# Optimization experiments

Hardware: AMD Instinct MI355X
Metric: run time of the kernel (lower is better)

## Reference

```python
import jax, jax.numpy as jnp
import numpy as np

D_PAIR = 128
D_BIAS = 128
N_HEAD = 4
D_HID = 32
B = 1
L = 384
EPS = 1e-5


def _layernorm(x, gamma, beta):
    m = jnp.mean(x, axis=-1, keepdims=True)
    v = jnp.var(x, axis=-1, keepdims=True)
    return (x - m) * jax.lax.rsqrt(v + EPS) * gamma + beta


def setup_inputs() -> dict:
    key = jax.random.key(0)
    ks = jax.random.split(key, 10)
    hd = N_HEAD * D_HID
    s = 0.02
    return {
        "pair": jax.random.normal(ks[0], (B, L, L, D_PAIR), jnp.float32),
        "bias": jax.random.normal(ks[1], (B, L, L, D_BIAS), jnp.float32),
        "gamma_p": jnp.ones((D_PAIR,), jnp.float32),
        "beta_p": jnp.zeros((D_PAIR,), jnp.float32),
        "gamma_b": jnp.ones((D_BIAS,), jnp.float32),
        "beta_b": jnp.zeros((D_BIAS,), jnp.float32),
        "Wq": jax.random.normal(ks[2], (D_PAIR, hd), jnp.float32) * s,
        "Wk": jax.random.normal(ks[3], (D_PAIR, hd), jnp.float32) * s,
        "Wv": jax.random.normal(ks[4], (D_PAIR, hd), jnp.float32) * s,
        "Wb": jax.random.normal(ks[5], (D_BIAS, N_HEAD), jnp.float32) * s,
        "Wg": jax.random.normal(ks[6], (D_PAIR, hd), jnp.float32) * s,
        "bg": jnp.ones((hd,), jnp.float32),
        "Wout": jax.random.normal(ks[7], (hd, D_PAIR), jnp.float32) * s,
        "bout": jnp.zeros((D_PAIR,), jnp.float32),
    }


def reference(pair, bias, gamma_p, beta_p, gamma_b, beta_b,
              Wq, Wk, Wv, Wb, Wg, bg, Wout, bout):
    h = Wb.shape[1]
    d = Wq.shape[1] // h
    Bn, Ln = pair.shape[:2]
    scaling = 1.0 / jnp.sqrt(jnp.asarray(d, pair.dtype))

    # is_row=True: attend along rows -> swap the two L axes
    pair_t = jnp.transpose(pair, (0, 2, 1, 3))
    bias_t = jnp.transpose(bias, (0, 2, 1, 3))

    pn = _layernorm(pair_t, gamma_p, beta_p)                     # [B,L,L,dp]
    q = (pn @ Wq).reshape(Bn, Ln, Ln, h, d) * scaling            # [B,n,i,h,d]
    k = (pn @ Wk).reshape(Bn, Ln, Ln, h, d) / Ln                 # [B,n,j,h,d]

    # mean-over-n biased axial attention logits: [B,i,j,h]
    attn = jnp.einsum('bnihk,bnjhk->bijh', q, k)
    attn = attn + _layernorm(bias_t, gamma_b, beta_b) @ Wb       # learned bias
    a = jax.nn.softmax(attn, axis=-2)                            # over j

    v = (pn @ Wv).reshape(Bn, Ln, Ln, h, d)                      # [B,n,j,h,d]
    o = jnp.einsum('bijh,bnjhd->bnihd', a, v).reshape(Bn, Ln, Ln, h * d)

    gate = jax.nn.sigmoid(pn @ Wg + bg)                          # [B,L,L,h*d]
    out = (gate * o) @ Wout + bout                               # [B,L,L,dp]

    return jnp.transpose(out, (0, 2, 1, 3))                      # undo is_row permute
```

## Files before the change

kernel.cpp:

```cpp
#include <hip/hip_runtime.h>

typedef unsigned short u16;
typedef unsigned int   u32;
typedef __attribute__((ext_vector_type(8))) short bf16x8;
typedef __attribute__((ext_vector_type(4))) float f32x4;

#define LL 384
#define DP 128
#define SZROW ((size_t)LL * LL)

#define SWZ(row, col) (((row) << 7) + (((((col) >> 3) ^ ((row) & 7)) << 3) | ((col) & 7)))

__device__ __forceinline__ u16 f2bf(float x) {
  u32 u = __builtin_bit_cast(u32, x);
  u = (u + 0x7FFFu + ((u >> 16) & 1u)) >> 16;
  return (u16)u;
}
__device__ __forceinline__ float bf2f(u16 h) {
  return __builtin_bit_cast(float, ((u32)h) << 16);
}
__device__ __forceinline__ uint2 pack4(float a, float b, float c, float d) {
  uint2 p;
  p.x = (u32)f2bf(a) | ((u32)f2bf(b) << 16);
  p.y = (u32)f2bf(c) | ((u32)f2bf(d) << 16);
  return p;
}


__global__ void k_prep(const float* __restrict__ Wq, const float* __restrict__ Wk,
                       const float* __restrict__ Wv, const float* __restrict__ Wg,
                       const float* __restrict__ Wout, u16* __restrict__ wbf) {
  int r = blockIdx.x, c = threadIdx.x, m = blockIdx.y;
  const float* W;
  float s = 1.0f;
  if (m == 0)      { W = Wq;  s = 0.17677669529663687f; }
  else if (m == 1) { W = Wk;  s = 1.0f / 384.0f; }
  else if (m == 2) { W = Wv; }
  else if (m == 3) { W = Wg; }
  else             { W = Wout; }
  wbf[m * DP * DP + r * DP + c] = f2bf(W[c * DP + r] * s);
}

template <int NS>
__device__ __forceinline__ void wave_gemm(const u16* __restrict__ W, const u16* pnl,
                                          int wave, int q, int r, f32x4 (&acc)[2][NS]) {
  const f32x4 FZ = {0.f, 0.f, 0.f, 0.f};
#pragma unroll
  for (int ms = 0; ms < 2; ++ms)
#pragma unroll
    for (int ns = 0; ns < NS; ++ns) acc[ms][ns] = FZ;
#pragma unroll
  for (int kc = 0; kc < 4; ++kc) {
    bf16x8 a0 = *(const bf16x8*)(W + (wave * 32 + r) * DP + kc * 32 + q * 8);
    bf16x8 a1 = *(const bf16x8*)(W + (wave * 32 + 16 + r) * DP + kc * 32 + q * 8);
#pragma unroll
    for (int ns = 0; ns < NS; ++ns) {
      bf16x8 b = *(const bf16x8*)(pnl + SWZ(ns * 16 + r, kc * 32 + q * 8));
      acc[0][ns] = __builtin_amdgcn_mfma_f32_16x16x32_bf16(a0, b, acc[0][ns], 0, 0, 0);
      acc[1][ns] = __builtin_amdgcn_mfma_f32_16x16x32_bf16(a1, b, acc[1][ns], 0, 0, 0);
    }
  }
}

__global__ __launch_bounds__(256) void k1_ln_proj(
    const float* __restrict__ pair, const float* __restrict__ gamma_p,
    const float* __restrict__ beta_p, const u16* __restrict__ wbf,
    const float* __restrict__ bg, u16* __restrict__ Qb, u16* __restrict__ Kb,
    u16* __restrict__ Vp, u16* __restrict__ Gtb) {
  __shared__ u16 pn[64 * 128];
  __shared__ u16 T[128 * 72];
  const int ib = blockIdx.x, n = blockIdx.y;
  const int tid = threadIdx.x;
  const int lane = tid & 63, wave = tid >> 6;
  const int q = lane >> 4, r = lane & 15;
  const int l32 = lane & 31, half = lane >> 5;
  const int c0 = l32 * 4;
  const float4 gm = *(const float4*)(gamma_p + c0);
  const float4 bt = *(const float4*)(beta_p + c0);

#pragma unroll
  for (int it = 0; it < 8; ++it) {
    const int il = it * 8 + wave * 2 + half;
    const float* rowp = pair + ((size_t)(ib * 64 + il) * LL + n) * DP + c0;
    float4 x = *(const float4*)rowp;
    float s1 = x.x + x.y + x.z + x.w;
    float s2 = x.x * x.x + x.y * x.y + x.z * x.z + x.w * x.w;
#pragma unroll
    for (int m = 16; m >= 1; m >>= 1) { s1 += __shfl_xor(s1, m); s2 += __shfl_xor(s2, m); }
    float mean = s1 * (1.0f / 128.0f);
    float rs = rsqrtf(s2 * (1.0f / 128.0f) - mean * mean + 1e-5f);
    *(uint2*)(&pn[SWZ(il, c0)]) =
        pack4((x.x - mean) * rs * gm.x + bt.x, (x.y - mean) * rs * gm.y + bt.y,
              (x.z - mean) * rs * gm.z + bt.z, (x.w - mean) * rs * gm.w + bt.w);
  }
  __syncthreads();

  f32x4 acc[2][4];

  wave_gemm<4>(wbf, pn, wave, q, r, acc);
#pragma unroll
  for (int ms = 0; ms < 2; ++ms) {
#pragma unroll
    for (int ns = 0; ns < 4; ++ns) {
      size_t base = (((size_t)n * 4 + wave) * LL + ib * 64 + ns * 16 + r) * 32 + ms * 16 + q * 4;
      *(uint2*)(Qb + base) = pack4(acc[ms][ns][0], acc[ms][ns][1], acc[ms][ns][2], acc[ms][ns][3]);
    }
  }
  wave_gemm<4>(wbf + DP * DP, pn, wave, q, r, acc);
#pragma unroll
  for (int ms = 0; ms < 2; ++ms) {
#pragma unroll
    for (int ns = 0; ns < 4; ++ns) {
      size_t base = (((size_t)n * 4 + wave) * LL + ib * 64 + ns * 16 + r) * 32 + ms * 16 + q * 4;
      *(uint2*)(Kb + base) = pack4(acc[ms][ns][0], acc[ms][ns][1], acc[ms][ns][2], acc[ms][ns][3]);
    }
  }
  wave_gemm<4>(wbf + 2 * DP * DP, pn, wave, q, r, acc);
#pragma unroll
  for (int ms = 0; ms < 2; ++ms)
#pragma unroll
    for (int ns = 0; ns < 4; ++ns)
#pragma unroll
      for (int reg = 0; reg < 4; ++reg)
        T[(wave * 32 + ms * 16 + q * 4 + reg) * 72 + ns * 16 + r] = f2bf(acc[ms][ns][reg]);
  __syncthreads();
#pragma unroll
  for (int kk = 0; kk < 2; ++kk) {
    u16* dst = Vp + ((size_t)n * 12 + ib * 2 + kk) * (128 * 32);
#pragma unroll
    for (int e = 0; e < 2; ++e) {
      int m = e * 256 + tid;
      int c = m >> 2, io = (m & 3) * 8;
      *(uint4*)(dst + c * 32 + io) = *(const uint4*)(T + c * 72 + kk * 32 + io);
    }
  }
  wave_gemm<4>(wbf + 3 * DP * DP, pn, wave, q, r, acc);
  __syncthreads();
#pragma unroll
  for (int ms = 0; ms < 2; ++ms) {
    f32x4 bgv = *(const f32x4*)(bg + wave * 32 + ms * 16 + q * 4);
#pragma unroll
    for (int ns = 0; ns < 4; ++ns)
#pragma unroll
      for (int reg = 0; reg < 4; ++reg) {
        float x = acc[ms][ns][reg] + bgv[reg];
        T[(wave * 32 + ms * 16 + q * 4 + reg) * 72 + ns * 16 + r] =
            f2bf(1.0f / (1.0f + __expf(-x)));
      }
  }
  __syncthreads();
#pragma unroll
  for (int it = 0; it < 4; ++it) {
    int c = it * 32 + (tid >> 3);
    int il2 = (tid & 7) * 8;
    *(uint4*)(Gtb + ((size_t)n * DP + c) * LL + ib * 64 + il2) =
        *(const uint4*)(T + c * 72 + il2);
  }
}

__global__ __launch_bounds__(256) void k2a_bias(
    const float* __restrict__ bias, const float* __restrict__ gamma_b,
    const float* __restrict__ beta_b, const float* __restrict__ Wb,
    float* __restrict__ part) {
  const int lane = threadIdx.x & 63, wave = threadIdx.x >> 6;
  const int l32 = lane & 31, half = lane >> 5;
  const int row = blockIdx.x * 8 + wave * 2 + half;
  const int i = row % LL, j = row / LL;
  const int c0 = l32 * 4;
  float4 x = *(const float4*)(bias + (size_t)row * DP + c0);
  float s1 = x.x + x.y + x.z + x.w;
  float s2 = x.x * x.x + x.y * x.y + x.z * x.z + x.w * x.w;
#pragma unroll
  for (int m = 16; m >= 1; m >>= 1) { s1 += __shfl_xor(s1, m); s2 += __shfl_xor(s2, m); }
  float mean = s1 * (1.0f / 128.0f);
  float rs = rsqrtf(s2 * (1.0f / 128.0f) - mean * mean + 1e-5f);
  const float4 gm = *(const float4*)(gamma_b + c0);
  const float4 bt = *(const float4*)(beta_b + c0);
  float y0 = (x.x - mean) * rs * gm.x + bt.x;
  float y1 = (x.y - mean) * rs * gm.y + bt.y;
  float y2 = (x.z - mean) * rs * gm.z + bt.z;
  float y3 = (x.w - mean) * rs * gm.w + bt.w;
  f32x4 w0 = *(const f32x4*)(Wb + (c0 + 0) * 4);
  f32x4 w1 = *(const f32x4*)(Wb + (c0 + 1) * 4);
  f32x4 w2 = *(const f32x4*)(Wb + (c0 + 2) * 4);
  f32x4 w3 = *(const f32x4*)(Wb + (c0 + 3) * 4);
  f32x4 pv = y0 * w0 + y1 * w1 + y2 * w2 + y3 * w3;
#pragma unroll
  for (int m = 16; m >= 1; m >>= 1) {
    pv[0] += __shfl_xor(pv[0], m); pv[1] += __shfl_xor(pv[1], m);
    pv[2] += __shfl_xor(pv[2], m); pv[3] += __shfl_xor(pv[3], m);
  }
  if (l32 == 0) {
    size_t o = (size_t)i * LL + j;
    part[(size_t)32 * SZROW + o] = pv[0];
    part[(size_t)33 * SZROW + o] = pv[1];
    part[(size_t)34 * SZROW + o] = pv[2];
    part[(size_t)35 * SZROW + o] = pv[3];
  }
}

__global__ __launch_bounds__(256) void k2b_qk(const u16* __restrict__ Qb,
                                              const u16* __restrict__ Kb,
                                              float* __restrict__ part) {
  const int it = blockIdx.y, jt = blockIdx.x >> 3, nc = blockIdx.x & 7;
  const int lane = threadIdx.x & 63, h = threadIdx.x >> 6;
  const int q = lane >> 4, r = lane & 15;
  const f32x4 FZ = {0.f, 0.f, 0.f, 0.f};
  f32x4 acc[3][3];
#pragma unroll
  for (int a = 0; a < 3; ++a)
#pragma unroll
    for (int b = 0; b < 3; ++b) acc[a][b] = FZ;
#pragma unroll 2
  for (int n = nc * 48; n < nc * 48 + 48; ++n) {
    const u16* Qp = Qb + (((size_t)n * 4 + h) * LL + it * 48 + r) * 32 + q * 8;
    const u16* Kp = Kb + (((size_t)n * 4 + h) * LL + jt * 48 + r) * 32 + q * 8;
    bf16x8 av[3], bv[3];
#pragma unroll
    for (int s = 0; s < 3; ++s) {
      av[s] = *(const bf16x8*)(Qp + s * 16 * 32);
      bv[s] = *(const bf16x8*)(Kp + s * 16 * 32);
    }
#pragma unroll
    for (int is = 0; is < 3; ++is)
#pragma unroll
      for (int js = 0; js < 3; ++js)
        acc[is][js] = __builtin_amdgcn_mfma_f32_16x16x32_bf16(av[is], bv[js], acc[is][js], 0, 0, 0);
  }
  float* dst = part + (size_t)(nc * 4 + h) * SZROW;
#pragma unroll
  for (int is = 0; is < 3; ++is)
#pragma unroll
    for (int js = 0; js < 3; ++js)
#pragma unroll
      for (int reg = 0; reg < 4; ++reg)
        dst[(size_t)(it * 48 + is * 16 + q * 4 + reg) * LL + jt * 48 + js * 16 + r] =
            acc[is][js][reg];
}

__global__ __launch_bounds__(384) void k3_softmax(const float* __restrict__ part,
                                                  u16* __restrict__ ap) {
  const int i = blockIdx.x, h = blockIdx.y, j = threadIdx.x;
  __shared__ float red[6];
  float l = 0.f;
#pragma unroll
  for (int c = 0; c < 9; ++c) l += part[(size_t)(c * 4 + h) * SZROW + (size_t)i * LL + j];
  float m = l;
#pragma unroll
  for (int s = 32; s >= 1; s >>= 1) m = fmaxf(m, __shfl_xor(m, s));
  const int wv = threadIdx.x >> 6;
  if ((threadIdx.x & 63) == 0) red[wv] = m;
  __syncthreads();
  m = fmaxf(fmaxf(fmaxf(red[0], red[1]), fmaxf(red[2], red[3])), fmaxf(red[4], red[5]));
  float e = __expf(l - m);
  float s = e;
#pragma unroll
  for (int t = 32; t >= 1; t >>= 1) s += __shfl_xor(s, t);
  __syncthreads();
  if ((threadIdx.x & 63) == 0) red[wv] = s;
  __syncthreads();
  s = red[0] + red[1] + red[2] + red[3] + red[4] + red[5];
  ap[(((size_t)h * 12 + (j >> 5)) * LL + i) * 32 + (j & 31)] = f2bf(e / s);
}

__global__ __launch_bounds__(256) void k4_out(
    const u16* __restrict__ ap, const u16* __restrict__ Vp,
    const u16* __restrict__ Gtb, const u16* __restrict__ Wot,
    const float* __restrict__ bout, float* __restrict__ out) {
  __shared__ __align__(16) char smem[64 * 132 * 4];
  u16*   go = (u16*)smem;
  float* O  = (float*)smem;
  const int n = blockIdx.x, ib = blockIdx.y;
  const int tid = threadIdx.x;
  const int lane = tid & 63, wave = tid >> 6;
  const int h = wave;
  const int q = lane >> 4, r = lane & 15;

  uint2 gp[4][2];
#pragma unroll
  for (int is = 0; is < 4; ++is)
#pragma unroll
    for (int ds = 0; ds < 2; ++ds) {
      int c = h * 32 + ds * 16 + r;
      gp[is][ds] =
          *(const uint2*)(Gtb + ((size_t)n * DP + c) * LL + ib * 64 + is * 16 + q * 4);
    }

  const f32x4 FZ = {0.f, 0.f, 0.f, 0.f};
  f32x4 acc[4][2];
#pragma unroll
  for (int is = 0; is < 4; ++is) { acc[is][0] = FZ; acc[is][1] = FZ; }

  const u16* Vbase = Vp + (size_t)n * 12 * (128 * 32) + (h * 32 + r) * 32 + q * 8;
  const u16* Abase = ap + ((size_t)h * 12 * LL + ib * 64 + r) * 32 + q * 8;

  bf16x8 av[2][4];
#pragma unroll
  for (int is = 0; is < 4; ++is) av[0][is] = *(const bf16x8*)(Abase + (size_t)is * 16 * 32);

#pragma unroll
  for (int halfk = 0; halfk < 2; ++halfk) {
    bf16x8 vb[6][2];
#pragma unroll
    for (int k2 = 0; k2 < 6; ++k2) {
      const u16* Vkc = Vbase + (size_t)(halfk * 6 + k2) * (128 * 32);
      vb[k2][0] = *(const bf16x8*)(Vkc);
      vb[k2][1] = *(const bf16x8*)(Vkc + 16 * 32);
    }
#pragma unroll
    for (int k2 = 0; k2 < 6; ++k2) {
      const int kc = halfk * 6 + k2;
      const int cur = kc & 1, nxt = cur ^ 1;
      if (kc < 11) {
        const u16* An = Abase + (size_t)(kc + 1) * LL * 32;
#pragma unroll
        for (int is = 0; is < 4; ++is) av[nxt][is] = *(const bf16x8*)(An + (size_t)is * 16 * 32);
      }
#pragma unroll
      for (int is = 0; is < 4; ++is) {
        acc[is][0] = __builtin_amdgcn_mfma_f32_16x16x32_bf16(av[cur][is], vb[k2][0], acc[is][0], 0, 0, 0);
        acc[is][1] = __builtin_amdgcn_mfma_f32_16x16x32_bf16(av[cur][is], vb[k2][1], acc[is][1], 0, 0, 0);
      }
    }
  }
#pragma unroll
  for (int is = 0; is < 4; ++is)
#pragma unroll
    for (int ds = 0; ds < 2; ++ds) {
      int c = h * 32 + ds * 16 + r;
      float g0 = bf2f((u16)(gp[is][ds].x & 0xffff)), g1 = bf2f((u16)(gp[is][ds].x >> 16));
      float g2 = bf2f((u16)(gp[is][ds].y & 0xffff)), g3 = bf2f((u16)(gp[is][ds].y >> 16));
      int il = is * 16 + q * 4;
      go[SWZ(il + 0, c)] = f2bf(g0 * acc[is][ds][0]);
      go[SWZ(il + 1, c)] = f2bf(g1 * acc[is][ds][1]);
      go[SWZ(il + 2, c)] = f2bf(g2 * acc[is][ds][2]);
      go[SWZ(il + 3, c)] = f2bf(g3 * acc[is][ds][3]);
    }
  __syncthreads();

  f32x4 acc2[2][4];
  wave_gemm<4>(Wot, go, wave, q, r, acc2);
  __syncthreads();

#pragma unroll
  for (int ms = 0; ms < 2; ++ms) {
    int co = wave * 32 + ms * 16 + q * 4;
    f32x4 bo = *(const f32x4*)(bout + co);
#pragma unroll
    for (int ns = 0; ns < 4; ++ns)
      *(f32x4*)(O + (ns * 16 + r) * 132 + co) = acc2[ms][ns] + bo;
  }
  __syncthreads();
#pragma unroll
  for (int e = 0; e < 8; ++e) {
    int m = e * 256 + tid;
    int il = m >> 5, cw = (m & 31) * 4;
    *(f32x4*)(out + ((size_t)(ib * 64 + il) * LL + n) * DP + cw) =
        *(const f32x4*)(O + il * 132 + cw);
  }
}

extern "C" void kernel_launch(void* const* d_in, const int* in_sizes, int n_in,
                              void* d_out, int out_size, void* d_ws, size_t ws_size,
                              hipStream_t stream) {
  const float* pair    = (const float*)d_in[0];
  const float* bias    = (const float*)d_in[1];
  const float* gamma_p = (const float*)d_in[2];
  const float* beta_p  = (const float*)d_in[3];
  const float* gamma_b = (const float*)d_in[4];
  const float* beta_b  = (const float*)d_in[5];
  const float* Wq      = (const float*)d_in[6];
  const float* Wk      = (const float*)d_in[7];
  const float* Wv      = (const float*)d_in[8];
  const float* Wb      = (const float*)d_in[9];
  const float* Wg      = (const float*)d_in[10];
  const float* bg      = (const float*)d_in[11];
  const float* Wout    = (const float*)d_in[12];
  const float* bout    = (const float*)d_in[13];

  u16* Qb = (u16*)d_out;
  u16* Kb = Qb + (size_t)LL * LL * DP;

  char* ws = (char*)d_ws;
  const size_t BF_PLANE = (size_t)LL * LL * DP * 2;
  u16*   Vp   = (u16*)ws;
  u16*   Gtb  = (u16*)(ws + BF_PLANE);
  float* part = (float*)(ws + 2 * BF_PLANE);
  u16*   ap   = (u16*)(ws + 2 * BF_PLANE + 36 * SZROW * 4);
  u16*   wbf  = (u16*)(ws + 2 * BF_PLANE + 36 * SZROW * 4 + 4 * SZROW * 2);
  float* out  = (float*)d_out;

  k_prep<<<dim3(128, 5), 128, 0, stream>>>(Wq, Wk, Wv, Wg, Wout, wbf);
  k1_ln_proj<<<dim3(6, 384), 256, 0, stream>>>(pair, gamma_p, beta_p, wbf, bg, Qb, Kb, Vp, Gtb);
  k2a_bias<<<dim3(18432), 256, 0, stream>>>(bias, gamma_b, beta_b, Wb, part);
  k2b_qk<<<dim3(64, 8), 256, 0, stream>>>(Qb, Kb, part);
  k3_softmax<<<dim3(384, 4), 384, 0, stream>>>(part, ap);
  k4_out<<<dim3(384, 6), 256, 0, stream>>>(ap, Vp, Gtb, wbf + 4 * DP * DP, bout, out);
}
```

Measured before the change: 395.9 us.

## Compute V and gate projections transposed to write outputs directly, skip LDS staging

```diff
diff --git a/kernel.cpp b/kernel.cpp
--- a/kernel.cpp
+++ b/kernel.cpp
@@ -62,36 +62,62 @@
   }
 }
 
+__device__ __forceinline__ void wave_gemm_t(const u16* __restrict__ W, const u16* pnl,
+                                            int wave, int q, int r, f32x4 (&acc)[8]) {
+  const f32x4 FZ = {0.f, 0.f, 0.f, 0.f};
+#pragma unroll
+  for (int cb = 0; cb < 8; ++cb) acc[cb] = FZ;
+#pragma unroll
+  for (int kc = 0; kc < 4; ++kc) {
+    bf16x8 a = *(const bf16x8*)(pnl + SWZ(wave * 16 + r, kc * 32 + q * 8));
+#pragma unroll
+    for (int cb = 0; cb < 8; ++cb) {
+      bf16x8 b = *(const bf16x8*)(W + (cb * 16 + r) * DP + kc * 32 + q * 8);
+      acc[cb] = __builtin_amdgcn_mfma_f32_16x16x32_bf16(a, b, acc[cb], 0, 0, 0);
+    }
+  }
+}
+
 __global__ __launch_bounds__(256) void k1_ln_proj(
     const float* __restrict__ pair, const float* __restrict__ gamma_p,
     const float* __restrict__ beta_p, const u16* __restrict__ wbf,
     const float* __restrict__ bg, u16* __restrict__ Qb, u16* __restrict__ Kb,
     u16* __restrict__ Vp, u16* __restrict__ Gtb) {
   __shared__ u16 pn[64 * 128];
-  __shared__ u16 T[128 * 72];
   const int ib = blockIdx.x, n = blockIdx.y;
   const int tid = threadIdx.x;
   const int lane = tid & 63, wave = tid >> 6;
   const int q = lane >> 4, r = lane & 15;
-  const int l32 = lane & 31, half = lane >> 5;
-  const int c0 = l32 * 4;
-  const float4 gm = *(const float4*)(gamma_p + c0);
-  const float4 bt = *(const float4*)(beta_p + c0);
-
-#pragma unroll
-  for (int it = 0; it < 8; ++it) {
-    const int il = it * 8 + wave * 2 + half;
+  const int sub = lane & 15, rw = lane >> 4;
+  const int c0 = sub * 8;
+  const float4 gmA = *(const float4*)(gamma_p + c0);
+  const float4 gmB = *(const float4*)(gamma_p + c0 + 4);
+  const float4 btA = *(const float4*)(beta_p + c0);
+  const float4 btB = *(const float4*)(beta_p + c0 + 4);
+
+#pragma unroll
+  for (int it = 0; it < 4; ++it) {
+    const int il = it * 16 + wave * 4 + rw;
     const float* rowp = pair + ((size_t)(ib * 64 + il) * LL + n) * DP + c0;
-    float4 x = *(const float4*)rowp;
-    float s1 = x.x + x.y + x.z + x.w;
-    float s2 = x.x * x.x + x.y * x.y + x.z * x.z + x.w * x.w;
-#pragma unroll
-    for (int m = 16; m >= 1; m >>= 1) { s1 += __shfl_xor(s1, m); s2 += __shfl_xor(s2, m); }
+    float4 xa = *(const float4*)rowp;
+    float4 xb = *(const float4*)(rowp + 4);
+    float s1 = xa.x + xa.y + xa.z + xa.w + xb.x + xb.y + xb.z + xb.w;
+    float s2 = xa.x * xa.x + xa.y * xa.y + xa.z * xa.z + xa.w * xa.w +
+               xb.x * xb.x + xb.y * xb.y + xb.z * xb.z + xb.w * xb.w;
+#pragma unroll
+    for (int m = 8; m >= 1; m >>= 1) { s1 += __shfl_xor(s1, m); s2 += __shfl_xor(s2, m); }
     float mean = s1 * (1.0f / 128.0f);
     float rs = rsqrtf(s2 * (1.0f / 128.0f) - mean * mean + 1e-5f);
-    *(uint2*)(&pn[SWZ(il, c0)]) =
-        pack4((x.x - mean) * rs * gm.x + bt.x, (x.y - mean) * rs * gm.y + bt.y,
-              (x.z - mean) * rs * gm.z + bt.z, (x.w - mean) * rs * gm.w + bt.w);
+    uint4 pk;
+    pk.x = (u32)f2bf((xa.x - mean) * rs * gmA.x + btA.x) |
+           ((u32)f2bf((xa.y - mean) * rs * gmA.y + btA.y) << 16);
+    pk.y = (u32)f2bf((xa.z - mean) * rs * gmA.z + btA.z) |
+           ((u32)f2bf((xa.w - mean) * rs * gmA.w + btA.w) << 16);
+    pk.z = (u32)f2bf((xb.x - mean) * rs * gmB.x + btB.x) |
+           ((u32)f2bf((xb.y - mean) * rs * gmB.y + btB.y) << 16);
+    pk.w = (u32)f2bf((xb.z - mean) * rs * gmB.z + btB.z) |
+           ((u32)f2bf((xb.w - mean) * rs * gmB.w + btB.w) << 16);
+    *(uint4*)(&pn[SWZ(il, c0)]) = pk;
   }
   __syncthreads();
 
@@ -115,46 +141,31 @@
       *(uint2*)(Kb + base) = pack4(acc[ms][ns][0], acc[ms][ns][1], acc[ms][ns][2], acc[ms][ns][3]);
     }
   }
-  wave_gemm<4>(wbf + 2 * DP * DP, pn, wave, q, r, acc);
-#pragma unroll
-  for (int ms = 0; ms < 2; ++ms)
-#pragma unroll
-    for (int ns = 0; ns < 4; ++ns)
-#pragma unroll
-      for (int reg = 0; reg < 4; ++reg)
-        T[(wave * 32 + ms * 16 + q * 4 + reg) * 72 + ns * 16 + r] = f2bf(acc[ms][ns][reg]);
-  __syncthreads();
-#pragma unroll
-  for (int kk = 0; kk < 2; ++kk) {
-    u16* dst = Vp + ((size_t)n * 12 + ib * 2 + kk) * (128 * 32);
-#pragma unroll
-    for (int e = 0; e < 2; ++e) {
-      int m = e * 256 + tid;
-      int c = m >> 2, io = (m & 3) * 8;
-      *(uint4*)(dst + c * 32 + io) = *(const uint4*)(T + c * 72 + kk * 32 + io);
-    }
-  }
-  wave_gemm<4>(wbf + 3 * DP * DP, pn, wave, q, r, acc);
-  __syncthreads();
-#pragma unroll
-  for (int ms = 0; ms < 2; ++ms) {
-    f32x4 bgv = *(const f32x4*)(bg + wave * 32 + ms * 16 + q * 4);
-#pragma unroll
-    for (int ns = 0; ns < 4; ++ns)
-#pragma unroll
-      for (int reg = 0; reg < 4; ++reg) {
-        float x = acc[ms][ns][reg] + bgv[reg];
-        T[(wave * 32 + ms * 16 + q * 4 + reg) * 72 + ns * 16 + r] =
-            f2bf(1.0f / (1.0f + __expf(-x)));
-      }
-  }
-  __syncthreads();
-#pragma unroll
-  for (int it = 0; it < 4; ++it) {
-    int c = it * 32 + (tid >> 3);
-    int il2 = (tid & 7) * 8;
-    *(uint4*)(Gtb + ((size_t)n * DP + c) * LL + ib * 64 + il2) =
-        *(const uint4*)(T + c * 72 + il2);
+  {
+    f32x4 acc2[8];
+    wave_gemm_t(wbf + 2 * DP * DP, pn, wave, q, r, acc2);
+    const int il0 = wave * 16 + q * 4;
+    u16* dst = Vp + ((size_t)n * 12 + ib * 2 + (il0 >> 5)) * (128 * 32) + (il0 & 31);
+#pragma unroll
+    for (int cb = 0; cb < 8; ++cb) {
+      int c = cb * 16 + r;
+      *(uint2*)(dst + c * 32) = pack4(acc2[cb][0], acc2[cb][1], acc2[cb][2], acc2[cb][3]);
+    }
+  }
+  {
+    f32x4 acc2[8];
+    wave_gemm_t(wbf + 3 * DP * DP, pn, wave, q, r, acc2);
+    const int il0 = wave * 16 + q * 4;
+#pragma unroll
+    for (int cb = 0; cb < 8; ++cb) {
+      int c = cb * 16 + r;
+      float bgc = bg[c];
+      float g0 = 1.0f / (1.0f + __expf(-(acc2[cb][0] + bgc)));
+      float g1 = 1.0f / (1.0f + __expf(-(acc2[cb][1] + bgc)));
+      float g2 = 1.0f / (1.0f + __expf(-(acc2[cb][2] + bgc)));
+      float g3 = 1.0f / (1.0f + __expf(-(acc2[cb][3] + bgc)));
+      *(uint2*)(Gtb + ((size_t)n * DP + c) * LL + ib * 64 + il0) = pack4(g0, g1, g2, g3);
+    }
   }
 }
 
@@ -163,34 +174,42 @@
     const float* __restrict__ beta_b, const float* __restrict__ Wb,
     float* __restrict__ part) {
   const int lane = threadIdx.x & 63, wave = threadIdx.x >> 6;
-  const int l32 = lane & 31, half = lane >> 5;
-  const int row = blockIdx.x * 8 + wave * 2 + half;
+  const int sub = lane & 15, rw = lane >> 4;
+  const int row = blockIdx.x * 16 + wave * 4 + rw;
   const int i = row % LL, j = row / LL;
-  const int c0 = l32 * 4;
-  float4 x = *(const float4*)(bias + (size_t)row * DP + c0);
-  float s1 = x.x + x.y + x.z + x.w;
-  float s2 = x.x * x.x + x.y * x.y + x.z * x.z + x.w * x.w;
-#pragma unroll
-  for (int m = 16; m >= 1; m >>= 1) { s1 += __shfl_xor(s1, m); s2 += __shfl_xor(s2, m); }
+  const int c0 = sub * 8;
+  const float* src = bias + (size_t)row * DP + c0;
+  float4 xa = *(const float4*)src;
+  float4 xb = *(const float4*)(src + 4);
+  float s1 = xa.x + xa.y + xa.z + xa.w + xb.x + xb.y + xb.z + xb.w;
+  float s2 = xa.x * xa.x + xa.y * xa.y + xa.z * xa.z + xa.w * xa.w +
+             xb.x * xb.x + xb.y * xb.y + xb.z * xb.z + xb.w * xb.w;
+#pragma unroll
+  for (int m = 8; m >= 1; m >>= 1) { s1 += __shfl_xor(s1, m); s2 += __shfl_xor(s2, m); }
   float mean = s1 * (1.0f / 128.0f);
   float rs = rsqrtf(s2 * (1.0f / 128.0f) - mean * mean + 1e-5f);
-  const float4 gm = *(const float4*)(gamma_b + c0);
-  const float4 bt = *(const float4*)(beta_b + c0);
-  float y0 = (x.x - mean) * rs * gm.x + bt.x;
-  float y1 = (x.y - mean) * rs * gm.y + bt.y;
-  float y2 = (x.z - mean) * rs * gm.z + bt.z;
-  float y3 = (x.w - mean) * rs * gm.w + bt.w;
-  f32x4 w0 = *(const f32x4*)(Wb + (c0 + 0) * 4);
-  f32x4 w1 = *(const f32x4*)(Wb + (c0 + 1) * 4);
-  f32x4 w2 = *(const f32x4*)(Wb + (c0 + 2) * 4);
-  f32x4 w3 = *(const f32x4*)(Wb + (c0 + 3) * 4);
-  f32x4 pv = y0 * w0 + y1 * w1 + y2 * w2 + y3 * w3;
-#pragma unroll
-  for (int m = 16; m >= 1; m >>= 1) {
+  const float4 gmA = *(const float4*)(gamma_b + c0);
+  const float4 gmB = *(const float4*)(gamma_b + c0 + 4);
+  const float4 btA = *(const float4*)(beta_b + c0);
+  const float4 btB = *(const float4*)(beta_b + c0 + 4);
+  float y[8];
+  y[0] = (xa.x - mean) * rs * gmA.x + btA.x;
+  y[1] = (xa.y - mean) * rs * gmA.y + btA.y;
+  y[2] = (xa.z - mean) * rs * gmA.z + btA.z;
+  y[3] = (xa.w - mean) * rs * gmA.w + btA.w;
+  y[4] = (xb.x - mean) * rs * gmB.x + btB.x;
+  y[5] = (xb.y - mean) * rs * gmB.y + btB.y;
+  y[6] = (xb.z - mean) * rs * gmB.z + btB.z;
+  y[7] = (xb.w - mean) * rs * gmB.w + btB.w;
+  f32x4 pv = {0.f, 0.f, 0.f, 0.f};
+#pragma unroll
+  for (int k = 0; k < 8; ++k) pv += y[k] * *(const f32x4*)(Wb + (c0 + k) * 4);
+#pragma unroll
+  for (int m = 8; m >= 1; m >>= 1) {
     pv[0] += __shfl_xor(pv[0], m); pv[1] += __shfl_xor(pv[1], m);
     pv[2] += __shfl_xor(pv[2], m); pv[3] += __shfl_xor(pv[3], m);
   }
-  if (l32 == 0) {
+  if (sub == 0) {
     size_t o = (size_t)i * LL + j;
     part[(size_t)32 * SZROW + o] = pv[0];
     part[(size_t)33 * SZROW + o] = pv[1];
@@ -392,7 +411,7 @@
 
   k_prep<<<dim3(128, 5), 128, 0, stream>>>(Wq, Wk, Wv, Wg, Wout, wbf);
   k1_ln_proj<<<dim3(6, 384), 256, 0, stream>>>(pair, gamma_p, beta_p, wbf, bg, Qb, Kb, Vp, Gtb);
-  k2a_bias<<<dim3(18432), 256, 0, stream>>>(bias, gamma_b, beta_b, Wb, part);
+  k2a_bias<<<dim3(9216), 256, 0, stream>>>(bias, gamma_b, beta_b, Wb, part);
   k2b_qk<<<dim3(64, 8), 256, 0, stream>>>(Qb, Kb, part);
   k3_softmax<<<dim3(384, 4), 384, 0, stream>>>(part, ap);
   k4_out<<<dim3(384, 6), 256, 0, stream>>>(ap, Vp, Gtb, wbf + 4 * DP * DP, bout, out);
```

New measurement: 445.2 us. +12.5%, slower.
